# Kernel optimization log

Measured on AMD Instinct MI355X. Metric: run time of the kernel, lower is better.

## Reference

```python
import jax, jax.numpy as jnp
import numpy as np

N, E, G = 20000, 320000, 256
F = 128
C = [256, 512, 1024]
NHID, NOUT = 1024, 768
EPS = 1e-5


def setup_inputs() -> dict:
    key = jax.random.key(0)
    keys = iter(jax.random.split(key, 64))
    def nrm(shape, s=0.02):
        return jax.random.normal(next(keys), shape, jnp.float32) * s
    inp = {}
    inp["x"] = jax.random.normal(next(keys), (N, F), jnp.float32)
    inp["edge_index"] = jax.random.randint(next(keys), (2, E), 0, N)
    inp["batch"] = jnp.sort(jax.random.randint(next(keys), (N,), 0, G))
    # stem GCNConv: F -> C[0]
    inp["w0"] = nrm((F, C[0])); inp["b0"] = jnp.zeros((C[0],), jnp.float32)
    # residual blocks
    for i in range(2):
        cin, cout = C[i], C[i + 1]
        mid = cin + (cout - cin) // 2
        p = f"blk{i}_"
        inp[p + "w1"] = nrm((cin, mid)); inp[p + "b1"] = jnp.zeros((mid,), jnp.float32)
        inp[p + "g1"] = jnp.ones((mid,), jnp.float32); inp[p + "be1"] = jnp.zeros((mid,), jnp.float32)
        inp[p + "w2"] = nrm((mid, cout)); inp[p + "b2"] = jnp.zeros((cout,), jnp.float32)
        inp[p + "g2"] = jnp.ones((cout,), jnp.float32); inp[p + "be2"] = jnp.zeros((cout,), jnp.float32)
        inp[p + "w3"] = nrm((cin, cout)); inp[p + "b3"] = jnp.zeros((cout,), jnp.float32)
    inp["mw1"] = nrm((C[-1], NHID)); inp["mb1"] = jnp.zeros((NHID,), jnp.float32)
    inp["mw2"] = nrm((NHID, NOUT)); inp["mb2"] = jnp.zeros((NOUT,), jnp.float32)
    return inp


def _gcn(x, w, b, src, dst, dinv):
    # PyG GCNConv: D^{-1/2}(A+I)D^{-1/2} X W + b, deg computed with self-loops
    xw = x @ w                                     # [N, Cout]
    msg = xw[src] * dinv[src, None]                # [E, Cout]
    agg = jax.ops.segment_sum(msg, dst, num_segments=x.shape[0])
    return agg * dinv[:, None] + xw * (dinv * dinv)[:, None] + b


def _bn(h, g, b):
    # BatchNorm1d in training mode: biased batch statistics over nodes
    m = h.mean(axis=0)
    v = h.var(axis=0)
    return g * (h - m) * jax.lax.rsqrt(v + EPS) + b


def reference(x, edge_index, batch, w0, b0,
              blk0_w1, blk0_b1, blk0_g1, blk0_be1, blk0_w2, blk0_b2, blk0_g2, blk0_be2, blk0_w3, blk0_b3,
              blk1_w1, blk1_b1, blk1_g1, blk1_be1, blk1_w2, blk1_b2, blk1_g2, blk1_be2, blk1_w3, blk1_b3,
              mw1, mb1, mw2, mb2):
    src, dst = edge_index[0], edge_index[1]
    deg = 1.0 + jax.ops.segment_sum(jnp.ones((src.shape[0],), x.dtype), dst, num_segments=x.shape[0])
    dinv = jax.lax.rsqrt(deg)                      # deg >= 1, no zero guard needed

    h = jax.nn.relu(_gcn(x, w0, b0, src, dst, dinv))
    blocks = [
        (blk0_w1, blk0_b1, blk0_g1, blk0_be1, blk0_w2, blk0_b2, blk0_g2, blk0_be2, blk0_w3, blk0_b3),
        (blk1_w1, blk1_b1, blk1_g1, blk1_be1, blk1_w2, blk1_b2, blk1_g2, blk1_be2, blk1_w3, blk1_b3),
    ]
    for (w1, b1, g1, be1, w2, b2, g2, be2, w3, b3) in blocks:
        t = jax.nn.relu(_bn(_gcn(h, w1, b1, src, dst, dinv), g1, be1))
        t = jax.nn.relu(_bn(_gcn(t, w2, b2, src, dst, dinv), g2, be2))
        h = jax.nn.relu(t) + _gcn(h, w3, b3, src, dst, dinv)

    # global mean pool over graphs
    s = jax.ops.segment_sum(h, batch, num_segments=G)
    cnt = jax.ops.segment_sum(jnp.ones((h.shape[0],), h.dtype), batch, num_segments=G)
    pooled = s / jnp.maximum(cnt, 1.0)[:, None]    # [G, C[-1]]

    out = jax.nn.relu(pooled @ mw1 + mb1) @ mw2 + mb2
    return out
```

## Files before the change

kernel.cpp:

```cpp
#include <hip/hip_runtime.h>
#include <cstdint>
#include <cstddef>

#define NN 20000
#define NE 320000
#define NG 256
#define NB 79
#define MBK 157

typedef unsigned short u16;
typedef __attribute__((ext_vector_type(8))) short bf16x8;
typedef __attribute__((ext_vector_type(4))) float f32x4;

__device__ inline float b2f(u16 h){
  union { unsigned u; float f; } v; v.u = ((unsigned)h) << 16; return v.f;
}
__device__ inline u16 f2b(float f){
  union { float f; unsigned u; } v; v.f = f;
  unsigned r = v.u + 0x7FFFu + ((v.u >> 16) & 1u);
  return (u16)(r >> 16);
}
__device__ inline void up8(const uint4& v, float* a){
  union { unsigned u; float f; } t;
  t.u = v.x << 16;         a[0] = t.f;
  t.u = v.x & 0xffff0000u; a[1] = t.f;
  t.u = v.y << 16;         a[2] = t.f;
  t.u = v.y & 0xffff0000u; a[3] = t.f;
  t.u = v.z << 16;         a[4] = t.f;
  t.u = v.z & 0xffff0000u; a[5] = t.f;
  t.u = v.w << 16;         a[6] = t.f;
  t.u = v.w & 0xffff0000u; a[7] = t.f;
}
__device__ inline unsigned pk2(float a, float b){
  return (unsigned)f2b(a) | (((unsigned)f2b(b)) << 16);
}

__device__ inline void gload_lds16(const void* g, void* l){
  __builtin_amdgcn_global_load_lds(
      (const __attribute__((address_space(1))) unsigned int*)g,
      (__attribute__((address_space(3))) unsigned int*)l, 16, 0, 0);
}


__global__ void k_zero(int* __restrict__ p, int n){
  int i = blockIdx.x*blockDim.x + threadIdx.x;
  if (i < n) p[i] = 0;
}

__global__ void k_deg(const int* __restrict__ ei, int* __restrict__ deg){
  int e = blockIdx.x*blockDim.x + threadIdx.x;
  if (e < NE) atomicAdd(&deg[ei[NE + e]], 1);
}

__global__ void k_scan1(const int* __restrict__ counts, int* __restrict__ bsum,
                        float* __restrict__ dinv){
  __shared__ int sm[256];
  int b = blockIdx.x, tid = threadIdx.x, idx = b*256 + tid;
  int v = (idx < NN) ? counts[idx] : 0;
  if (idx < NN) dinv[idx] = rsqrtf(1.0f + (float)v);
  sm[tid] = v;
  __syncthreads();
  for (int d = 128; d > 0; d >>= 1){
    if (tid < d) sm[tid] += sm[tid + d];
    __syncthreads();
  }
  if (tid == 0) bsum[b] = sm[0];
}
__global__ void k_scan2(int* __restrict__ bsum){
  if (threadIdx.x == 0){
    int c = 0;
    for (int i = 0; i < NB; i++){ int t = bsum[i]; bsum[i] = c; c += t; }
    bsum[NB] = c;
  }
}
__global__ void k_scan3(const int* __restrict__ counts, const int* __restrict__ bsum,
                        int* __restrict__ offs){
  __shared__ int sm[256];
  int b = blockIdx.x, tid = threadIdx.x, idx = b*256 + tid;
  int v = (idx < NN) ? counts[idx] : 0;
  sm[tid] = v;
  __syncthreads();
  for (int d = 1; d < 256; d <<= 1){
    int t = (tid >= d) ? sm[tid - d] : 0;
    __syncthreads();
    sm[tid] += t;
    __syncthreads();
  }
  if (idx < NN) offs[idx] = bsum[b] + sm[tid] - v;
  if (idx == NN - 1) offs[NN] = bsum[NB];
}

__global__ void k_fill(const int* __restrict__ ei, const int* __restrict__ offs,
                       int* __restrict__ cur, int* __restrict__ srcs){
  int e = blockIdx.x*blockDim.x + threadIdx.x;
  if (e < NE){
    int s = ei[e];
    int d = ei[NE + e];
    int p = atomicAdd(&cur[d], 1);
    srcs[offs[d] + p] = s;
  }
}

__global__ void k_bounds(const int* __restrict__ batch, int* __restrict__ start){
  int i = blockIdx.x*blockDim.x + threadIdx.x;
  if (i < NN){
    int b  = batch[i];
    int bp = (i == 0) ? -1 : batch[i-1];
    for (int g = bp + 1; g <= b; g++) start[g] = i;
    if (i == NN - 1){
      for (int g = b + 1; g <= NG; g++) start[g] = NN;
    }
  }
}

__global__ void k_cast(const float* __restrict__ x, uint4* __restrict__ xb,
                       const float* __restrict__ dinv, int total16){
  int t = blockIdx.x*blockDim.x + threadIdx.x;
  if (t >= total16) return;
  int i = t >> 4;
  int c = t & 15;
  float di = dinv[i];
  const float* xp = x + (size_t)i*128 + c*8;
  float4 a = *(const float4*)xp;
  float4 b = *(const float4*)(xp + 4);
  uint4 o;
  o.x = pk2(a.x*di, a.y*di); o.y = pk2(a.z*di, a.w*di);
  o.z = pk2(b.x*di, b.y*di); o.w = pk2(b.z*di, b.w*di);
  int g = c >> 1, cl = c & 1;
  xb[(size_t)g*NN*2 + (size_t)i*2 + cl] = o;
}

struct WPArgs {
  const float* w[7];
  u16* wt[7];
  int K[7], N[7];
  int tstart[8];
};
__global__ __launch_bounds__(256) void k_wprep7(WPArgs a){
  __shared__ float sm[64][65];
  int bid = blockIdx.x;
  int wi = 0;
  while (wi < 6 && bid >= a.tstart[wi+1]) wi++;
  int tt = bid - a.tstart[wi];
  int K = a.K[wi], N = a.N[wi];
  int nk = K >> 6;
  int kb = (tt % nk) * 64, nb = (tt / nk) * 64;
  const float* w = a.w[wi];
  u16* wt = a.wt[wi];
  int tid = threadIdx.x;
  #pragma unroll
  for (int i = 0; i < 16; i++){
    int t = i*256 + tid;
    int r = t >> 6, c = t & 63;
    sm[r][c] = w[(size_t)(kb + r) * N + nb + c];
  }
  __syncthreads();
  #pragma unroll
  for (int i = 0; i < 16; i++){
    int t = i*256 + tid;
    int r = t >> 6, c = t & 63;
    wt[(size_t)(nb + r) * K + kb + c] = f2b(sm[c][r]);
  }
}

__global__ __launch_bounds__(256) void k_bncoef(const float* __restrict__ pst,
                        const float* __restrict__ gam, const float* __restrict__ bet,
                        float* __restrict__ scsh, int Nc){
  __shared__ float red[2][8][32];
  int ci = threadIdx.x & 31;
  int ms = threadIdx.x >> 5;
  int c = blockIdx.x * 32 + ci;
  float S = 0.f, S2 = 0.f;
  for (int m = ms; m < MBK*2; m += 8){
    S  += pst[((size_t)m*2 + 0)*Nc + c];
    S2 += pst[((size_t)m*2 + 1)*Nc + c];
  }
  red[0][ms][ci] = S; red[1][ms][ci] = S2;
  __syncthreads();
  if (ms == 0){
    #pragma unroll
    for (int k = 1; k < 8; k++){ S += red[0][k][ci]; S2 += red[1][k][ci]; }
    float mean = S * (1.0f / NN);
    float var  = S2 * (1.0f / NN) - mean*mean;
    float rs = rsqrtf(var + 1e-5f);
    float sc = gam[c] * rs;
    scsh[c] = sc;
    scsh[Nc + c] = bet[c] - mean * sc;
  }
}

template<int C8>
__global__ __launch_bounds__(256) void k_bnscale(const uint4* __restrict__ src,
                        uint4* __restrict__ dst,
                        const float* __restrict__ dinv,
                        const float* __restrict__ scsh){
  constexpr int C8G = C8 / 8;
  constexpr int C = C8 * 8;
  int t = blockIdx.x*blockDim.x + threadIdx.x;
  if (t >= NN * C8) return;
  int i = t / C8;
  int c = t - i * C8;
  float sc[8], sh[8];
  #pragma unroll
  for (int k = 0; k < 8; k++){
    int ch = c*8 + k;
    sc[k] = scsh[ch];
    sh[k] = scsh[C + ch];
  }
  float di = dinv[i];
  float a[8];
  up8(src[t], a);
  #pragma unroll
  for (int k = 0; k < 8; k++) a[k] = fmaxf(fmaf(a[k], sc[k], sh[k]), 0.f) * di;
  uint4 o;
  o.x = pk2(a[0], a[1]); o.y = pk2(a[2], a[3]);
  o.z = pk2(a[4], a[5]); o.w = pk2(a[6], a[7]);
  int g = c / C8G, cl = c - g * C8G;
  dst[(size_t)g*NN*C8G + (size_t)i*C8G + cl] = o;
}

template<int C8, int C8G>
__global__ __launch_bounds__(256) void k_agg_b(const uint4* __restrict__ in, uint4* __restrict__ out,
                        const float* __restrict__ dinv, const int* __restrict__ offs,
                        const int* __restrict__ srcs){
  int bid = blockIdx.x;
  int g = bid & 7;
  int t = (bid >> 3)*256 + threadIdx.x;
  if (t >= NN * C8G) return;
  int i = t / C8G;
  int cl = t - i * C8G;
  const uint4* base = in + (size_t)g*NN*C8G + cl;
  float acc[8];
  up8(base[(size_t)i * C8G], acc);
  int e = offs[i], e1 = offs[i + 1];
  for (; e + 4 <= e1; e += 4){
    int sA = srcs[e], sB = srcs[e+1], sC = srcs[e+2], sD = srcs[e+3];
    uint4 yA = base[(size_t)sA * C8G];
    uint4 yB = base[(size_t)sB * C8G];
    uint4 yC = base[(size_t)sC * C8G];
    uint4 yD = base[(size_t)sD * C8G];
    float b[8];
    up8(yA, b);
    #pragma unroll
    for (int k = 0; k < 8; k++) acc[k] += b[k];
    up8(yB, b);
    #pragma unroll
    for (int k = 0; k < 8; k++) acc[k] += b[k];
    up8(yC, b);
    #pragma unroll
    for (int k = 0; k < 8; k++) acc[k] += b[k];
    up8(yD, b);
    #pragma unroll
    for (int k = 0; k < 8; k++) acc[k] += b[k];
  }
  for (; e < e1; e++){
    int s = srcs[e];
    float b[8];
    up8(base[(size_t)s * C8G], b);
    #pragma unroll
    for (int k = 0; k < 8; k++) acc[k] += b[k];
  }
  float di = dinv[i];
  #pragma unroll
  for (int k = 0; k < 8; k++) acc[k] *= di;
  uint4 o;
  o.x = pk2(acc[0], acc[1]); o.y = pk2(acc[2], acc[3]);
  o.z = pk2(acc[4], acc[5]); o.w = pk2(acc[6], acc[7]);
  out[(size_t)i * C8 + g * C8G + cl] = o;
}

template<int MODE, bool STATS, bool SCALE, bool BLK>
__global__ __launch_bounds__(256, 4) void k_mfma(const u16* __restrict__ A,
                                                 const u16* __restrict__ BT,
                                                 const float* __restrict__ bias,
                                                 const u16* __restrict__ C,
                                                 u16* __restrict__ Co,
                                                 float* __restrict__ pst,
                                                 const float* __restrict__ scsh,
                                                 const float* __restrict__ dv,
                                                 int M, int K, int Nc){
  __shared__ u16 S[128*128];
  u16* As = S;
  u16* Bs = S + 128*64;
  const int tid = threadIdx.x;
  const int lane = tid & 63;
  const int quad = lane >> 4;
  const int l16 = lane & 15;
  const int wid = tid >> 6;
  const int wm = wid & 1, wn = wid >> 1;

  const int nwg = gridDim.x * gridDim.y;
  const int p = blockIdx.y * gridDim.x + blockIdx.x;
  const int xcd = p & 7;
  const int q = nwg >> 3, r = nwg & 7;
  const int w = (xcd < r ? xcd * (q + 1) : r * (q + 1) + (xcd - r) * q) + (p >> 3);
  const int bn = (w % gridDim.x) * 128;
  const int bm = (w / gridDim.x) * 128;

  f32x4 acc[4][4];
  #pragma unroll
  for (int i = 0; i < 4; i++)
    #pragma unroll
    for (int j = 0; j < 4; j++)
      acc[i][j] = (f32x4){0.f, 0.f, 0.f, 0.f};

  const int srow = tid >> 3;
  const int scol8 = tid & 7;
  for (int k0 = 0; k0 < K; k0 += 64){
    #pragma unroll
    for (int i = 0; i < 4; i++){
      int row = i*32 + srow;
      int gc = (scol8 ^ (row & 7)) * 8;
      int lofs = row*64 + scol8*8;
      gload_lds16(A + (size_t)(bm + row) * K + k0 + gc, As + lofs);
      gload_lds16(BT + (size_t)(bn + row) * K + k0 + gc, Bs + lofs);
    }
    __syncthreads();
    #pragma unroll
    for (int kk = 0; kk < 2; kk++){
      const int col8 = kk*4 + quad;
      bf16x8 af[4], bfr[4];
      #pragma unroll
      for (int mi = 0; mi < 4; mi++){
        int row = wm*64 + mi*16 + l16;
        af[mi] = *(const bf16x8*)(As + row*64 + ((col8 ^ (row & 7)) * 8));
      }
      #pragma unroll
      for (int ni = 0; ni < 4; ni++){
        int row = wn*64 + ni*16 + l16;
        bfr[ni] = *(const bf16x8*)(Bs + row*64 + ((col8 ^ (row & 7)) * 8));
      }
      #pragma unroll
      for (int mi = 0; mi < 4; mi++)
        #pragma unroll
        for (int ni = 0; ni < 4; ni++)
          acc[mi][ni] = __builtin_amdgcn_mfma_f32_16x16x32_bf16(af[mi], bfr[ni], acc[mi][ni], 0, 0, 0);
    }
    __syncthreads();
  }
  #pragma unroll
  for (int ni = 0; ni < 4; ni++){
    int colL = wn*64 + ni*16 + l16;
    float bb = bias[bn + colL];
    float s = 0.f, s2 = 0.f;
    #pragma unroll
    for (int mi = 0; mi < 4; mi++){
      int rbase = wm*64 + mi*16 + quad*4;
      #pragma unroll
      for (int r2 = 0; r2 < 4; r2++){
        int rowL = rbase + r2;
        float v = acc[mi][ni][r2] + bb;
        if (STATS && (bm + rowL) < M){ s += v; s2 += v * v; }
        if (MODE == 1) v = fmaxf(v, 0.f);
        S[rowL*128 + colL] = f2b(v);
      }
    }
    if (STATS){
      s  += __shfl_xor(s, 16, 64);  s  += __shfl_xor(s, 32, 64);
      s2 += __shfl_xor(s2, 16, 64); s2 += __shfl_xor(s2, 32, 64);
      if (quad == 0){
        int mb = bm >> 7;
        size_t bi = ((size_t)(mb*2 + wm)*2)*Nc + bn + colL;
        pst[bi] = s;
        pst[bi + Nc] = s2;
      }
    }
  }
  __syncthreads();
  #pragma unroll
  for (int it = 0; it < 8; it++){
    int idx = it*256 + tid;
    int rl = idx >> 4, cq = idx & 15;
    int row = bm + rl;
    if (row < M){
      int col0 = bn + cq*8;
      uint4 wv = *(const uint4*)(S + rl*128 + cq*8);
      uint4 ou;
      if (MODE == 3){
        float di = SCALE ? dv[row] : 1.f;
        float o[8], ov[8];
        up8(wv, o);
        uint4 old = *(const uint4*)(C + (size_t)row * Nc + col0);
        up8(old, ov);
        #pragma unroll
        for (int k = 0; k < 8; k++){
          int ch = col0 + k;
          float sc = scsh[ch];
          float sh = scsh[Nc + ch];
          o[k] += fmaxf(fmaf(ov[k], sc, sh), 0.f);
          if (SCALE) o[k] *= di;
        }
        ou.x = pk2(o[0], o[1]); ou.y = pk2(o[2], o[3]);
        ou.z = pk2(o[4], o[5]); ou.w = pk2(o[6], o[7]);
      } else if (SCALE){
        float di = dv[row];
        float o[8];
        up8(wv, o);
        #pragma unroll
        for (int k = 0; k < 8; k++) o[k] *= di;
        ou.x = pk2(o[0], o[1]); ou.y = pk2(o[2], o[3]);
        ou.z = pk2(o[4], o[5]); ou.w = pk2(o[6], o[7]);
      } else {
        ou = wv;
      }
      if (BLK){
        int chpg = Nc >> 3;
        int g = col0 / chpg;
        int c8g = chpg >> 3;
        int cl = (col0 - g * chpg) >> 3;
        *((uint4*)Co + (size_t)g*NN*c8g + (size_t)row*c8g + cl) = ou;
      } else {
        *(uint4*)(Co + (size_t)row * Nc + col0) = ou;
      }
    }
  }
}

template<bool RELUA>
__global__ __launch_bounds__(256) void k_gemm_sk(const float* __restrict__ A,
                                                 const float* __restrict__ B,
                                                 float* __restrict__ Cp,
                                                 int M, int K, int Nc){
  __shared__ float As[16][68];
  __shared__ float Bs[16][64];
  const int tid = threadIdx.x;
  const int tx = tid & 15, ty = tid >> 4;
  const int bm = blockIdx.x * 64, bn = blockIdx.y * 64;
  const int kchunk = K / gridDim.z;
  const int ks = blockIdx.z * kchunk, ke = ks + kchunk;
  const int arow = tid >> 2, akq = (tid & 3) << 2;
  const int brow = tid >> 4, bcol = (tid & 15) << 2;
  float acc[4][4] = {{0.f}};
  const bool aval = (bm + arow) < M;
  const float* Aptr = A + (size_t)(bm + arow) * K + akq;
  const float* Bptr = B + (size_t)brow * Nc + bn + bcol;
  for (int k0 = ks; k0 < ke; k0 += 16){
    float4 av = make_float4(0.f, 0.f, 0.f, 0.f);
    if (aval) av = *(const float4*)(Aptr + k0);
    if (RELUA){
      av.x = fmaxf(av.x, 0.f); av.y = fmaxf(av.y, 0.f);
      av.z = fmaxf(av.z, 0.f); av.w = fmaxf(av.w, 0.f);
    }
    float4 bv = *(const float4*)(Bptr + (size_t)k0 * Nc);
    As[akq + 0][arow] = av.x;
    As[akq + 1][arow] = av.y;
    As[akq + 2][arow] = av.z;
    As[akq + 3][arow] = av.w;
    *(float4*)&Bs[brow][bcol] = bv;
    __syncthreads();
    #pragma unroll
    for (int kk = 0; kk < 16; kk++){
      const float4 a = *(const float4*)(&As[kk][ty << 2]);
      const float4 b = *(const float4*)(&Bs[kk][tx << 2]);
      const float ar[4] = {a.x, a.y, a.z, a.w};
      const float br[4] = {b.x, b.y, b.z, b.w};
      #pragma unroll
      for (int i = 0; i < 4; i++)
        #pragma unroll
        for (int j = 0; j < 4; j++)
          acc[i][j] = fmaf(ar[i], br[j], acc[i][j]);
    }
    __syncthreads();
  }
  const int col = bn + (tx << 2);
  float* base = Cp + (size_t)blockIdx.z * M * Nc;
  #pragma unroll
  for (int i = 0; i < 4; i++){
    int row = bm + (ty << 2) + i;
    if (row < M){
      *(float4*)(base + (size_t)row * Nc + col) =
          make_float4(acc[i][0], acc[i][1], acc[i][2], acc[i][3]);
    }
  }
}

template<int SPLITS>
__global__ __launch_bounds__(256) void k_redsk(const float4* __restrict__ part,
                                               const float* __restrict__ bias,
                                               float4* __restrict__ out,
                                               int M, int Nc4){
  int t = blockIdx.x*blockDim.x + threadIdx.x;
  int total = M * Nc4;
  if (t >= total) return;
  int col4 = t % Nc4;
  float4 s = ((const float4*)bias)[col4];
  #pragma unroll
  for (int z = 0; z < SPLITS; z++){
    float4 v = part[(size_t)z * total + t];
    s.x += v.x; s.y += v.y; s.z += v.z; s.w += v.w;
  }
  out[t] = s;
}

__global__ __launch_bounds__(256) void k_pool_b(const u16* __restrict__ h,
                                                const int* __restrict__ start,
                                                float* __restrict__ pooled){
  __shared__ float sm[128*8];
  int g = blockIdx.x;
  int half = threadIdx.x >> 7;
  int cb = threadIdx.x & 127;
  int c = cb << 3;
  int r0 = start[g], r1 = start[g + 1];
  float acc[8] = {0.f,0.f,0.f,0.f,0.f,0.f,0.f,0.f};
  for (int r = r0 + half; r < r1; r += 2){
    float b[8];
    up8(*(const uint4*)(h + (size_t)r * 1024 + c), b);
    #pragma unroll
    for (int k = 0; k < 8; k++) acc[k] += b[k];
  }
  if (half){
    #pragma unroll
    for (int k = 0; k < 8; k++) sm[cb*8 + k] = acc[k];
  }
  __syncthreads();
  if (!half){
    float inv = (r1 > r0) ? (1.0f / (float)(r1 - r0)) : 0.0f;
    float o[8];
    #pragma unroll
    for (int k = 0; k < 8; k++) o[k] = (acc[k] + sm[cb*8 + k]) * inv;
    float4* dst = (float4*)(pooled + (size_t)g * 1024 + c);
    dst[0] = make_float4(o[0], o[1], o[2], o[3]);
    dst[1] = make_float4(o[4], o[5], o[6], o[7]);
  }
}


extern "C" void kernel_launch(void* const* d_in, const int* in_sizes, int n_in,
                              void* d_out, int out_size, void* d_ws, size_t ws_size,
                              hipStream_t stream) {
  const float* x    = (const float*)d_in[0];
  const int*   ei   = (const int*)d_in[1];
  const int*   bat  = (const int*)d_in[2];
  const float* w0   = (const float*)d_in[3];
  const float* b0   = (const float*)d_in[4];
  const float* a_w1 = (const float*)d_in[5],  *a_b1  = (const float*)d_in[6];
  const float* a_g1 = (const float*)d_in[7],  *a_be1 = (const float*)d_in[8];
  const float* a_w2 = (const float*)d_in[9],  *a_b2  = (const float*)d_in[10];
  const float* a_g2 = (const float*)d_in[11], *a_be2 = (const float*)d_in[12];
  const float* a_w3 = (const float*)d_in[13], *a_b3  = (const float*)d_in[14];
  const float* c_w1 = (const float*)d_in[15], *c_b1  = (const float*)d_in[16];
  const float* c_g1 = (const float*)d_in[17], *c_be1 = (const float*)d_in[18];
  const float* c_w2 = (const float*)d_in[19], *c_b2  = (const float*)d_in[20];
  const float* c_g2 = (const float*)d_in[21], *c_be2 = (const float*)d_in[22];
  const float* c_w3 = (const float*)d_in[23], *c_b3  = (const float*)d_in[24];
  const float* mw1  = (const float*)d_in[25], *mb1   = (const float*)d_in[26];
  const float* mw2  = (const float*)d_in[27], *mb2   = (const float*)d_in[28];
  float* out = (float*)d_out;

  char* pp = (char*)d_ws;
  auto alloc = [&](size_t b)->char*{ char* r = pp; pp += (b + 255) & ~(size_t)255; return r; };

  const size_t CH = (size_t)NN * 2;
  char* R = alloc(2304 * CH);
  float* dinv = (float*)alloc((size_t)NN * 4);
  int* icomb  = (int*)alloc((size_t)2 * NN * 4);
  int* deg    = icomb;
  int* cur    = icomb + NN;
  int* offs   = (int*)alloc((size_t)(NN + 1) * 4);
  int* bsum   = (int*)alloc((size_t)(NB + 1) * 4);
  int* srcs   = (int*)alloc((size_t)NE * 4);
  int* startg = (int*)alloc((size_t)(NG + 1) * 4);
  float* SB   = (float*)alloc(5376 * 4);
  float* sA1 = SB;
  float* sA2 = SB + 768;
  float* sC1 = SB + 1792;
  float* sC2 = SB + 3328;
  float* pstat = (float*)alloc((size_t)MBK * 2 * 2 * 1024 * 4);
  u16* WT  = (u16*)alloc(2162688 * 2);
  u16* wt0  = WT;
  u16* wtA1 = WT + 32768;
  u16* wtA2 = WT + 131072;
  u16* wtA3 = WT + 327680;
  u16* wtC1 = WT + 458752;
  u16* wtC2 = WT + 851968;
  u16* wtC3 = WT + 1638400;
  float* P  = (float*)WT;
  float* Hh = P + (size_t)NG * 1024;

  auto slot = [&](int s)->u16*{ return (u16*)(R + (size_t)s * CH); };
  u16* xb    = slot(0);
  u16* ax    = slot(128);
  u16* h0    = slot(256);
  u16* ah0   = slot(512);
  u16* t1raw = slot(768);
  u16* t1b   = slot(1152);
  u16* at    = slot(1536);
  u16* h1raw = slot(0);
  u16* h1b   = slot(768);
  u16* ah1   = slot(1792);
  u16* u1raw = slot(0);
  u16* u1b   = slot(768);
  u16* au    = slot(0);
  u16* h2    = slot(768);
  float* part1 = (float*)slot(0);
  float* part2 = (float*)slot(256);

  auto cdiv = [](int a, int b){ return (a + b - 1) / b; };

  k_zero<<<cdiv(2*NN,256),256,0,stream>>>(icomb, 2*NN);
  k_deg <<<cdiv(NE,256),256,0,stream>>>(ei, deg);
  k_scan1<<<NB,256,0,stream>>>(deg, bsum, dinv);
  k_scan2<<<1,64,0,stream>>>(bsum);
  k_scan3<<<NB,256,0,stream>>>(deg, bsum, offs);
  k_fill<<<cdiv(NE,256),256,0,stream>>>(ei, offs, cur, srcs);
  k_bounds<<<cdiv(NN,256),256,0,stream>>>(bat, startg);
  k_cast<<<cdiv(NN*16,256),256,0,stream>>>(x, (uint4*)xb, dinv, NN*16);

  {
    WPArgs wa;
    const float* ws[7] = {w0, a_w1, a_w2, a_w3, c_w1, c_w2, c_w3};
    u16* wts[7] = {wt0, wtA1, wtA2, wtA3, wtC1, wtC2, wtC3};
    int Ks[7] = {128, 256, 384, 256, 512, 768, 512};
    int Ns[7] = {256, 384, 512, 512, 768, 1024, 1024};
    int acc = 0;
    for (int i = 0; i < 7; i++){
      wa.w[i] = ws[i]; wa.wt[i] = wts[i]; wa.K[i] = Ks[i]; wa.N[i] = Ns[i];
      wa.tstart[i] = acc;
      acc += (Ks[i]/64) * (Ns[i]/64);
    }
    wa.tstart[7] = acc;
    k_wprep7<<<acc,256,0,stream>>>(wa);
  }

  auto agg = [&](const u16* in, u16* o, int C){
    int C8 = C / 8;
    int C8G = C8 / 8;
    int gb = 8 * cdiv(NN * C8G, 256);
    switch (C8){
      case 16: k_agg_b<16, 2><<<gb,256,0,stream>>>((const uint4*)in,(uint4*)o,dinv,offs,srcs); break;
      case 32: k_agg_b<32, 4><<<gb,256,0,stream>>>((const uint4*)in,(uint4*)o,dinv,offs,srcs); break;
      case 48: k_agg_b<48, 6><<<gb,256,0,stream>>>((const uint4*)in,(uint4*)o,dinv,offs,srcs); break;
      case 64: k_agg_b<64, 8><<<gb,256,0,stream>>>((const uint4*)in,(uint4*)o,dinv,offs,srcs); break;
      case 96: k_agg_b<96,12><<<gb,256,0,stream>>>((const uint4*)in,(uint4*)o,dinv,offs,srcs); break;
      default: break;
    }
  };
  auto gemm0 = [&](const u16* A, const u16* BT_, const float* bi, u16* Cc,
                   int K, int Nc){
    dim3 g(Nc/128, cdiv(NN,128));
    k_mfma<0,true,false,false><<<g,256,0,stream>>>(A, BT_, bi, Cc, Cc, pstat, nullptr, dinv, NN, K, Nc);
  };
  auto bncoef = [&](const float* gm, const float* bt, float* scsh, int Nc){
    k_bncoef<<<Nc/32,256,0,stream>>>(pstat, gm, bt, scsh, Nc);
  };
  auto gemm1b = [&](const u16* A, const u16* BT_, const float* bi, u16* Cob,
                    int K, int Nc){
    dim3 g(Nc/128, cdiv(NN,128));
    k_mfma<1,false,true,true><<<g,256,0,stream>>>(A, BT_, bi, Cob, Cob, nullptr, nullptr, dinv, NN, K, Nc);
  };
  auto gemm3b = [&](const u16* A, const u16* BT_, const float* bi, const u16* Cold, u16* Cob,
                    int K, int Nc, const float* scsh){
    dim3 g(Nc/128, cdiv(NN,128));
    k_mfma<3,false,true,true><<<g,256,0,stream>>>(A, BT_, bi, Cold, Cob, nullptr, scsh, dinv, NN, K, Nc);
  };
  auto gemm3 = [&](const u16* A, const u16* BT_, const float* bi, u16* Cc,
                   int K, int Nc, const float* scsh){
    dim3 g(Nc/128, cdiv(NN,128));
    k_mfma<3,false,false,false><<<g,256,0,stream>>>(A, BT_, bi, Cc, Cc, nullptr, scsh, dinv, NN, K, Nc);
  };

  agg(xb, ax, 128);
  gemm1b(ax, wt0, b0, h0, 128, 256);
  agg(h0, ah0, 256);
  gemm0(ah0, wtA1, a_b1, t1raw, 256, 384);
  bncoef(a_g1, a_be1, sA1, 384);
  k_bnscale<48><<<cdiv(NN*48,256),256,0,stream>>>((const uint4*)t1raw, (uint4*)t1b, dinv, sA1);
  agg(t1b, at, 384);
  gemm0(at, wtA2, a_b2, h1raw, 384, 512);
  bncoef(a_g2, a_be2, sA2, 512);
  gemm3b(ah0, wtA3, a_b3, h1raw, h1b, 256, 512, sA2);
  agg(h1b, ah1, 512);
  gemm0(ah1, wtC1, c_b1, u1raw, 512, 768);
  bncoef(c_g1, c_be1, sC1, 768);
  k_bnscale<96><<<cdiv(NN*96,256),256,0,stream>>>((const uint4*)u1raw, (uint4*)u1b, dinv, sC1);
  agg(u1b, au, 768);
  gemm0(au, wtC2, c_b2, h2, 768, 1024);
  bncoef(c_g2, c_be2, sC2, 1024);
  gemm3(ah1, wtC3, c_b3, h2, 512, 1024, sC2);
  k_pool_b<<<NG,256,0,stream>>>(h2, startg, P);
  {
    dim3 g1(cdiv(NG,64), 1024/64, 8);
    k_gemm_sk<false><<<g1,256,0,stream>>>(P, mw1, part1, NG, 1024, 1024);
    k_redsk<8><<<cdiv(NG*256,256),256,0,stream>>>((const float4*)part1, mb1, (float4*)Hh, NG, 256);
    dim3 g2(cdiv(NG,64), 768/64, 8);
    k_gemm_sk<true><<<g2,256,0,stream>>>(Hh, mw2, part2, NG, 1024, 768);
    k_redsk<8><<<cdiv(NG*192,256),256,0,stream>>>((const float4*)part2, mb2, (float4*)out, NG, 192);
  }
}
```

Before: 576.5 us.

## Store aggregation output in channel-group-major layout and read it blocked in GEMM

The gather-aggregation kernel now writes its output in a channel-group-major layout ([group][node][C8G]) rather than row-major, so each channel group's writes are contiguous across nodes. The MFMA GEMM gains a CPG template parameter and computes A-tile addresses for this blocked layout when loading into LDS. This aims to improve write locality in the aggregation, at the cost of more scattered, strided A-operand reads in the GEMM. The helper lambdas are inlined into explicit launches.

```diff
diff --git a/kernel.cpp b/kernel.cpp
--- a/kernel.cpp
+++ b/kernel.cpp
@@ -266,10 +266,10 @@
   uint4 o;
   o.x = pk2(acc[0], acc[1]); o.y = pk2(acc[2], acc[3]);
   o.z = pk2(acc[4], acc[5]); o.w = pk2(acc[6], acc[7]);
-  out[(size_t)i * C8 + g * C8G + cl] = o;
-}
-
-template<int MODE, bool STATS, bool SCALE, bool BLK>
+  out[(size_t)g*NN*C8G + (size_t)i*C8G + cl] = o;
+}
+
+template<int MODE, bool STATS, bool SCALE, bool BLK, int CPG>
 __global__ __launch_bounds__(256, 4) void k_mfma(const u16* __restrict__ A,
                                                  const u16* __restrict__ BT,
                                                  const float* __restrict__ bias,
@@ -310,10 +310,13 @@
     #pragma unroll
     for (int i = 0; i < 4; i++){
       int row = i*32 + srow;
-      int gc = (scol8 ^ (row & 7)) * 8;
+      int gcc = scol8 ^ (row & 7);
       int lofs = row*64 + scol8*8;
-      gload_lds16(A + (size_t)(bm + row) * K + k0 + gc, As + lofs);
-      gload_lds16(BT + (size_t)(bn + row) * K + k0 + gc, Bs + lofs);
+      int q8 = (k0 >> 3) + gcc;
+      int gg = q8 / CPG;
+      int lq = q8 - gg * CPG;
+      gload_lds16(A + (((size_t)gg*NN + (bm + row))*CPG + lq)*8, As + lofs);
+      gload_lds16(BT + (size_t)(bn + row) * K + k0 + gcc*8, Bs + lofs);
     }
     __syncthreads();
     #pragma unroll
@@ -635,48 +638,32 @@
       default: break;
     }
   };
-  auto gemm0 = [&](const u16* A, const u16* BT_, const float* bi, u16* Cc,
-                   int K, int Nc){
-    dim3 g(Nc/128, cdiv(NN,128));
-    k_mfma<0,true,false,false><<<g,256,0,stream>>>(A, BT_, bi, Cc, Cc, pstat, nullptr, dinv, NN, K, Nc);
-  };
-  auto bncoef = [&](const float* gm, const float* bt, float* scsh, int Nc){
-    k_bncoef<<<Nc/32,256,0,stream>>>(pstat, gm, bt, scsh, Nc);
-  };
-  auto gemm1b = [&](const u16* A, const u16* BT_, const float* bi, u16* Cob,
-                    int K, int Nc){
-    dim3 g(Nc/128, cdiv(NN,128));
-    k_mfma<1,false,true,true><<<g,256,0,stream>>>(A, BT_, bi, Cob, Cob, nullptr, nullptr, dinv, NN, K, Nc);
-  };
-  auto gemm3b = [&](const u16* A, const u16* BT_, const float* bi, const u16* Cold, u16* Cob,
-                    int K, int Nc, const float* scsh){
-    dim3 g(Nc/128, cdiv(NN,128));
-    k_mfma<3,false,true,true><<<g,256,0,stream>>>(A, BT_, bi, Cold, Cob, nullptr, scsh, dinv, NN, K, Nc);
-  };
-  auto gemm3 = [&](const u16* A, const u16* BT_, const float* bi, u16* Cc,
-                   int K, int Nc, const float* scsh){
-    dim3 g(Nc/128, cdiv(NN,128));
-    k_mfma<3,false,false,false><<<g,256,0,stream>>>(A, BT_, bi, Cc, Cc, nullptr, scsh, dinv, NN, K, Nc);
-  };
 
   agg(xb, ax, 128);
-  gemm1b(ax, wt0, b0, h0, 128, 256);
+  { dim3 g(256/128, cdiv(NN,128));
+    k_mfma<1,false,true,true,2><<<g,256,0,stream>>>(ax, wt0, b0, h0, h0, nullptr, nullptr, dinv, NN, 128, 256); }
   agg(h0, ah0, 256);
-  gemm0(ah0, wtA1, a_b1, t1raw, 256, 384);
-  bncoef(a_g1, a_be1, sA1, 384);
+  { dim3 g(384/128, cdiv(NN,128));
+    k_mfma<0,true,false,false,4><<<g,256,0,stream>>>(ah0, wtA1, a_b1, t1raw, t1raw, pstat, nullptr, dinv, NN, 256, 384); }
+  k_bncoef<<<384/32,256,0,stream>>>(pstat, a_g1, a_be1, sA1, 384);
   k_bnscale<48><<<cdiv(NN*48,256),256,0,stream>>>((const uint4*)t1raw, (uint4*)t1b, dinv, sA1);
   agg(t1b, at, 384);
-  gemm0(at, wtA2, a_b2, h1raw, 384, 512);
-  bncoef(a_g2, a_be2, sA2, 512);
-  gemm3b(ah0, wtA3, a_b3, h1raw, h1b, 256, 512, sA2);
+  { dim3 g(512/128, cdiv(NN,128));
+    k_mfma<0,true,false,false,6><<<g,256,0,stream>>>(at, wtA2, a_b2, h1raw, h1raw, pstat, nullptr, dinv, NN, 384, 512); }
+  k_bncoef<<<512/32,256,0,stream>>>(pstat, a_g2, a_be2, sA2, 512);
+  { dim3 g(512/128, cdiv(NN,128));
+    k_mfma<3,false,true,true,4><<<g,256,0,stream>>>(ah0, wtA3, a_b3, h1raw, h1b, nullptr, sA2, dinv, NN, 256, 512); }
   agg(h1b, ah1, 512);
-  gemm0(ah1, wtC1, c_b1, u1raw, 512, 768);
-  bncoef(c_g1, c_be1, sC1, 768);
+  { dim3 g(768/128, cdiv(NN,128));
+    k_mfma<0,true,false,false,8><<<g,256,0,stream>>>(ah1, wtC1, c_b1, u1raw, u1raw, pstat, nullptr, dinv, NN, 512, 768); }
+  k_bncoef<<<768/32,256,0,stream>>>(pstat, c_g1, c_be1, sC1, 768);
   k_bnscale<96><<<cdiv(NN*96,256),256,0,stream>>>((const uint4*)u1raw, (uint4*)u1b, dinv, sC1);
   agg(u1b, au, 768);
-  gemm0(au, wtC2, c_b2, h2, 768, 1024);
-  bncoef(c_g2, c_be2, sC2, 1024);
-  gemm3(ah1, wtC3, c_b3, h2, 512, 1024, sC2);
+  { dim3 g(1024/128, cdiv(NN,128));
+    k_mfma<0,true,false,false,12><<<g,256,0,stream>>>(au, wtC2, c_b2, h2, h2, pstat, nullptr, dinv, NN, 768, 1024); }
+  k_bncoef<<<1024/32,256,0,stream>>>(pstat, c_g2, c_be2, sC2, 1024);
+  { dim3 g(1024/128, cdiv(NN,128));
+    k_mfma<3,false,false,false,8><<<g,256,0,stream>>>(ah1, wtC3, c_b3, h2, h2, nullptr, sC2, dinv, NN, 512, 1024); }
   k_pool_b<<<NG,256,0,stream>>>(h2, startg, P);
   {
     dim3 g1(cdiv(NG,64), 1024/64, 8);
```

New measurement: 585.8 us. No clear change (+1.6%).
